# Optimization experiments

Measured on AMD Instinct MI355X. Metric: run time of the kernel, lower is better.

The kernel has to match this reference:

```python
import jax, jax.numpy as jnp
import numpy as np
from jax import lax

SIZE = 4      # pool stride / patch stride
PAD = 1       # patch halo -> window = SIZE + 2*PAD = 6
K1 = 5        # mask mixing kernel
TOPK = 240    # hard-coded number of refinement regions per batch element


def conv2d(x, w, b, pad):
    # x: [B,Cin,H,W], w: [Cout,Cin,kh,kw] (torch OIHW layout)
    y = lax.conv_general_dilated(x, w, (1, 1), [(pad, pad), (pad, pad)],
                                 dimension_numbers=("NCHW", "OIHW", "NCHW"))
    return y + b[None, :, None, None]


def setup_inputs() -> dict:
    key = jax.random.key(0)
    ks = jax.random.split(key, 7)
    B, C, H, W = 16, 50, 256, 256
    out_lr = jax.random.normal(ks[0], (B, C, H, W), dtype=jnp.float32)
    s = 0.05  # keep conv outputs / softmax numerics sane
    return {
        "out_lr": out_lr,
        "W1": jax.random.normal(ks[1], (C, C, 3, 3), jnp.float32) * s,
        "b1": jax.random.normal(ks[2], (C,), jnp.float32) * s,
        "W2": jax.random.normal(ks[3], (2, C, 3, 3), jnp.float32) * s,
        "b2": jax.random.normal(ks[4], (2,), jnp.float32) * s,
        "Wk": jax.random.normal(ks[5], (K1 * K1, 1, 1, 1), jnp.float32) * s,
        "bk": jax.random.normal(ks[6], (K1 * K1,), jnp.float32) * s,
    }


def reference(out_lr, W1, b1, W2, b2, Wk, bk):
    B, C, H, W = out_lr.shape
    Hs, Ws = H // SIZE, W // SIZE

    # spa_mask_1 Sequential: conv3x3 -> ReLU -> conv3x3 (nf -> 2 channels)
    x = jax.nn.relu(conv2d(out_lr, W1, b1, 1))
    x = conv2d(x, W2, b2, 1)                      # [B,2,H,W]

    # softmax_t over channel dim (t=1), keep channel 1
    sm = jax.nn.softmax(x, axis=1)[:, 1:2]        # [B,1,H,W]

    # adaptive_avg_pool2d to (H/4, W/4) == 4x4 avg pool (H,W divisible by SIZE)
    sm = sm.reshape(B, 1, Hs, SIZE, Ws, SIZE).mean(axis=(3, 5))  # [B,1,Hs,Ws]
    sm = jnp.where(sm >= 0, sm, 0.1 * sm)         # LeakyReLU(0.1)

    # 1x1 conv producing per-position 5x5 mixing kernel
    kern = conv2d(sm, Wk, bk, 0)[:, None]         # [B,1,25,Hs,Ws]

    # F.unfold(pad=2, kernel 5x5): 25 sliding windows in row-major (ki,kj) order
    p = (K1 - 1) // 2
    smp = jnp.pad(sm, ((0, 0), (0, 0), (p, p), (p, p)))
    windows = jnp.stack([smp[:, :, i:i + Hs, j:j + Ws]
                         for i in range(K1) for j in range(K1)], axis=2)  # [B,1,25,Hs,Ws]

    final_mask = (kern * windows).sum(axis=2)     # [B,1,Hs,Ws]

    # topk 240 per batch; scatter->nonzero in torch yields row-major sorted flat indices
    err = final_mask.reshape(B, Hs * Ws)
    _, idx = lax.top_k(err, TOPK)                 # [B,240]
    idx = jnp.sort(idx, axis=1)
    b_idx = jnp.repeat(jnp.arange(B), TOPK)       # [B*240]
    flat = idx.reshape(-1)
    h_idx = flat // Ws
    w_idx = flat % Ws

    # crop_patch: pad by 1, gather 6x6 patches at stride 4 (direct gather, no full unfold)
    padded = jnp.pad(out_lr, ((0, 0), (0, 0), (PAD, PAD), (PAD, PAD)))
    win = SIZE + 2 * PAD

    def get_patch(b, h, w):
        return lax.dynamic_slice(padded, (b, 0, h * SIZE, w * SIZE), (1, C, win, win))[0]

    patches = jax.vmap(get_patch)(b_idx, h_idx, w_idx)  # [B*240, C, 6, 6]
    return patches, b_idx, h_idx, w_idx, final_mask
```

## Files before the change

### kernel.cpp

```cpp
#include <hip/hip_runtime.h>
#include <math.h>

#define CCH   50
#define HH    256
#define WW    256
#define BATCH 16
#define HSZ   64
#define WSZ   64
#define NTOP  240
#define SPX   66
#define SROW  6

typedef __attribute__((ext_vector_type(8))) short s16x8;
typedef __attribute__((ext_vector_type(4))) float f32x4;

__device__ __forceinline__ unsigned short bf16rne(float x) {
  unsigned u = __float_as_uint(x);
  unsigned r = (u + 0x7FFFu + ((u >> 16) & 1u)) >> 16;
  return (unsigned short)r;
}
__device__ __forceinline__ float bf2f(unsigned short h) {
  return __uint_as_float(((unsigned)h) << 16);
}

__global__ __launch_bounds__(64) void prep_wfrag_k(
    const float* __restrict__ W1, unsigned short* __restrict__ wf) {
  int combo = blockIdx.x;
  int lane = threadIdx.x;
  int sp = combo & 1;
  int t2 = combo >> 1;
  int mt = t2 & 3;
  int t3 = t2 >> 2;
  int tap = t3 % 9;
  int chunk = t3 / 9;
  int co = mt * 16 + (lane & 15);
  int gbase = combo * 512 + lane * 8;
#pragma unroll
  for (int e = 0; e < 8; ++e) {
    int ci = chunk * 32 + ((lane >> 4) * 8) + e;
    float w = (co < CCH && ci < CCH) ? W1[co * (CCH * 9) + ci * 9 + tap] : 0.f;
    unsigned short h = bf16rne(w);
    unsigned short v = sp ? bf16rne(w - bf2f(h)) : h;
    wf[gbase + e] = v;
  }
}

__global__ __launch_bounds__(256, 3) void conv1_mfma_k(
    const float* __restrict__ in, const unsigned short* __restrict__ wf,
    const float* __restrict__ b1, float* __restrict__ x1p) {
  __shared__ alignas(16) short xlds[SROW * SPX * 64];

  int bx = blockIdx.x;
  int pq = bx & 3;
  int rg = (bx >> 2) & 63;
  int b  = bx >> 8;
  int row0 = rg * 4;
  int px0g = pq * 64;

  int t = threadIdx.x;
  int lane = t & 63;
  int wv = t >> 6;
  int ln15 = lane & 15;
  int lg = lane >> 4;

  f32x4 acc[4][4];
#pragma unroll
  for (int mt = 0; mt < 4; ++mt)
#pragma unroll
    for (int s = 0; s < 4; ++s) acc[mt][s] = (f32x4){0.f, 0.f, 0.f, 0.f};

  const size_t in_b = ((size_t)b * CCH) << 16;

#pragma unroll
  for (int chunk = 0; chunk < 2; ++chunk) {
    __syncthreads();
    for (int i = t; i < SROW * 4 * SPX; i += 256) {
      int ro = i / SPX;
      int px = i - ro * SPX;
      int row = ro >> 2, oct = ro & 3;
      int gr = row0 - 1 + row;
      int gx = px0g - 1 + px;
      bool okxy = (gr >= 0 && gr < HH && gx >= 0 && gx < WW);
      const float* gp = in + in_b + ((size_t)(chunk * 32 + oct * 8) << 16)
                        + (gr << 8) + gx;
      unsigned hs[8], ls[8];
#pragma unroll
      for (int e = 0; e < 8; ++e) {
        int ci = chunk * 32 + oct * 8 + e;
        float x = (okxy && ci < CCH) ? gp[(size_t)e << 16] : 0.f;
        unsigned u = __float_as_uint(x);
        unsigned hu = u & 0xFFFF0000u;
        float lo = x - __uint_as_float(hu);
        unsigned ul = __float_as_uint(lo);
        hs[e] = hu >> 16;
        ls[e] = (ul + 0x7FFFu + ((ul >> 16) & 1u)) >> 16;
      }
      s16x8 hv, lv;
#pragma unroll
      for (int e = 0; e < 8; ++e) { hv[e] = (short)hs[e]; lv[e] = (short)ls[e]; }
      int swz = (px & 7) << 3;
      int base_sh = (row * SPX + px) * 64;
      *(s16x8*)&xlds[base_sh + ((oct * 8) ^ swz)] = hv;
      *(s16x8*)&xlds[base_sh + ((32 + oct * 8) ^ swz)] = lv;
    }
    __syncthreads();

#pragma unroll
    for (int tap = 0; tap < 9; ++tap) {
      const int dh = tap / 3 - 1;
      const int dw = tap % 3 - 1;
      s16x8 ah[4], al[4];
#pragma unroll
      for (int mt = 0; mt < 4; ++mt) {
        int cb = ((chunk * 9 + tap) * 4 + mt) * 2;
        ah[mt] = *(const s16x8*)(wf + (size_t)cb * 512 + lane * 8);
        al[mt] = *(const s16x8*)(wf + (size_t)(cb + 1) * 512 + lane * 8);
      }
      int rbase = (wv + 1 + dh) * (SPX * 64);
#pragma unroll
      for (int s = 0; s < 4; ++s) {
        int pixL = 1 + s * 16 + ln15 + dw;
        int bsh = rbase + pixL * 64;
        int swz = (pixL & 7) << 3;
        s16x8 bh = *(const s16x8*)&xlds[bsh + ((lg * 8) ^ swz)];
        s16x8 bl = *(const s16x8*)&xlds[bsh + ((32 + lg * 8) ^ swz)];
        __builtin_amdgcn_s_setprio(1);
#pragma unroll
        for (int mt = 0; mt < 4; ++mt) {
          acc[mt][s] = __builtin_amdgcn_mfma_f32_16x16x32_bf16(
              ah[mt], bh, acc[mt][s], 0, 0, 0);
          acc[mt][s] = __builtin_amdgcn_mfma_f32_16x16x32_bf16(
              ah[mt], bl, acc[mt][s], 0, 0, 0);
          acc[mt][s] = __builtin_amdgcn_mfma_f32_16x16x32_bf16(
              al[mt], bh, acc[mt][s], 0, 0, 0);
        }
        __builtin_amdgcn_s_setprio(0);
      }
    }
  }

  int orow = row0 + wv;
#pragma unroll
  for (int s = 0; s < 4; ++s) {
    int px = px0g + s * 16 + ln15;
#pragma unroll
    for (int mt = 0; mt < 4; ++mt) {
#pragma unroll
      for (int reg = 0; reg < 4; ++reg) {
        int co = mt * 16 + lg * 4 + reg;
        if (co < CCH) {
          float v = fmaxf(acc[mt][s][reg] + b1[co], 0.f);
          x1p[(((size_t)b * CCH + co) << 16) + (orow << 8) + px] = v;
        }
      }
    }
  }
}

__global__ __launch_bounds__(256) void conv2_pool_k(
    const float* __restrict__ x1p, const float* __restrict__ w2,
    const float* __restrict__ b2, float* __restrict__ pool) {
  int pb = blockIdx.x;
  int l = (pb & 7) * 128 + (pb >> 3);
  int b  = l >> 6;
  int rg = l & 63;
  int row0 = rg * 4;
  int px = threadIdx.x;

  float a0, a1, a2, a3, c0, c1, c2, c3;
  a0 = a1 = a2 = a3 = b2[0];
  c0 = c1 = c2 = c3 = b2[1];
  bool wm = px > 0, wp = px < WW - 1;

  const float* xb = x1p + (((size_t)b * CCH) << 16);

#define TAP(T, A, C) { \
    A = fmaf(wc0[3 * (T)], lf, A); A = fmaf(wc0[3 * (T) + 1], m, A); \
    A = fmaf(wc0[3 * (T) + 2], rt, A); \
    C = fmaf(wc1[3 * (T)], lf, C); C = fmaf(wc1[3 * (T) + 1], m, C); \
    C = fmaf(wc1[3 * (T) + 2], rt, C); }

#define ROW(IR, BODY) { \
    int gr = row0 - 1 + (IR); \
    if (gr >= 0 && gr < HH) { \
      const float* rp = xp + (gr << 8); \
      float m  = rp[px]; \
      float lf = wm ? rp[px - 1] : 0.f; \
      float rt = wp ? rp[px + 1] : 0.f; \
      BODY \
    } }

  for (int ci = 0; ci < CCH; ++ci) {
    const float* xp = xb + ((size_t)ci << 16);
    const float* wc0 = w2 + ci * 9;
    const float* wc1 = w2 + 450 + ci * 9;
    ROW(0, TAP(0, a0, c0))
    ROW(1, TAP(0, a1, c1) TAP(1, a0, c0))
    ROW(2, TAP(0, a2, c2) TAP(1, a1, c1) TAP(2, a0, c0))
    ROW(3, TAP(0, a3, c3) TAP(1, a2, c2) TAP(2, a1, c1))
    ROW(4, TAP(1, a3, c3) TAP(2, a2, c2))
    ROW(5, TAP(2, a3, c3))
  }
#undef ROW
#undef TAP

  float s = 1.f / (1.f + expf(a0 - c0)) + 1.f / (1.f + expf(a1 - c1))
          + 1.f / (1.f + expf(a2 - c2)) + 1.f / (1.f + expf(a3 - c3));
  s += __shfl_xor(s, 1);
  s += __shfl_xor(s, 2);
  if ((px & 3) == 0) {
    float p = s * (1.f / 16.f);
    pool[(size_t)b * 4096 + rg * 64 + (px >> 2)] = (p >= 0.f) ? p : 0.1f * p;
  }
}

__global__ __launch_bounds__(1024) void mixtopk_k(
    const float* __restrict__ pool, const float* __restrict__ wk,
    const float* __restrict__ bk, float* __restrict__ mask_out,
    float* __restrict__ ob, float* __restrict__ oh, float* __restrict__ ow,
    int* __restrict__ idx_ws) {
  __shared__ unsigned long long keys[4096];
  __shared__ int sidx[256];
  int b = blockIdx.x, t = threadIdx.x;

  const float* pb = pool + (size_t)b * 4096;
  for (int i = t; i < 4096; i += 1024) {
    int hs = i >> 6, ws = i & 63;
    float c = pb[i];
    float s = 0.f;
#pragma unroll
    for (int ki = 0; ki < 5; ++ki) {
#pragma unroll
      for (int kj = 0; kj < 5; ++kj) {
        int y = hs + ki - 2, x = ws + kj - 2;
        float win = (y >= 0 && y < HSZ && x >= 0 && x < WSZ)
                        ? pb[y * WSZ + x] : 0.f;
        int k = ki * 5 + kj;
        s += (wk[k] * c + bk[k]) * win;
      }
    }
    mask_out[(size_t)b * 4096 + i] = s;
    unsigned u = __float_as_uint(s);
    u = (u & 0x80000000u) ? ~u : (u | 0x80000000u);
    u = ~u;
    keys[i] = ((unsigned long long)u << 12) | (unsigned)i;
  }
  __syncthreads();

  for (int k = 2; k <= 4096; k <<= 1) {
    for (int j = k >> 1; j > 0; j >>= 1) {
      for (int m = t; m < 2048; m += 1024) {
        int i = ((m & ~(j - 1)) << 1) | (m & (j - 1));
        int l = i | j;
        bool up = ((i & k) == 0);
        unsigned long long a = keys[i], c = keys[l];
        if ((a > c) == up) { keys[i] = c; keys[l] = a; }
      }
      __syncthreads();
    }
  }

  if (t < 256) sidx[t] = (t < NTOP) ? (int)(keys[t] & 0xFFFu) : 0x7FFFFFFF;
  __syncthreads();
  for (int k = 2; k <= 256; k <<= 1) {
    for (int j = k >> 1; j > 0; j >>= 1) {
      if (t < 128) {
        int i = ((t & ~(j - 1)) << 1) | (t & (j - 1));
        int l = i | j;
        bool up = ((i & k) == 0);
        int a = sidx[i], c = sidx[l];
        if ((a > c) == up) { sidx[i] = c; sidx[l] = a; }
      }
      __syncthreads();
    }
  }

  if (t < NTOP) {
    int id = sidx[t];
    int o = b * NTOP + t;
    ob[o] = (float)b;
    oh[o] = (float)(id >> 6);
    ow[o] = (float)(id & 63);
    idx_ws[o] = id;
  }
}

__global__ __launch_bounds__(256) void gather_patch_k(
    const float* __restrict__ in, const int* __restrict__ idx_ws,
    float* __restrict__ patches) {
  int p = blockIdx.x;
  int b = p / NTOP;
  int id = idx_ws[p];
  int h = id >> 6, w = id & 63;
  int y0 = h * 4 - 1, x0 = w * 4 - 1;
  const float* base = in + (size_t)b * CCH * 65536;
  float* op = patches + (size_t)p * (CCH * 36);
  for (int e = threadIdx.x; e < CCH * 36; e += 256) {
    int c = e / 36;
    int r = (e - c * 36) / 6;
    int col = e - c * 36 - r * 6;
    int y = y0 + r, x = x0 + col;
    float v = 0.f;
    if (y >= 0 && y < HH && x >= 0 && x < WW)
      v = base[(size_t)c * 65536 + y * WW + x];
    op[e] = v;
  }
}

extern "C" void kernel_launch(void* const* d_in, const int* in_sizes, int n_in,
                              void* d_out, int out_size, void* d_ws, size_t ws_size,
                              hipStream_t stream) {
  const float* out_lr = (const float*)d_in[0];
  const float* W1 = (const float*)d_in[1];
  const float* b1 = (const float*)d_in[2];
  const float* W2 = (const float*)d_in[3];
  const float* b2 = (const float*)d_in[4];
  const float* Wk = (const float*)d_in[5];
  const float* bk = (const float*)d_in[6];

  float* x1p  = (float*)d_ws;
  float* pool = x1p + (size_t)52428800;
  int*  idxb  = (int*)(pool + 65536);
  unsigned short* wfrag = (unsigned short*)(pool + 65536 + 3840);

  float* out    = (float*)d_out;
  float* o_patch = out;
  float* o_b    = out + (size_t)6912000;
  float* o_h    = o_b + 3840;
  float* o_w    = o_h + 3840;
  float* o_mask = o_w + 3840;

  prep_wfrag_k<<<144, 64, 0, stream>>>(W1, wfrag);
  conv1_mfma_k<<<BATCH * 64 * 4, 256, 0, stream>>>(out_lr, wfrag, b1, x1p);
  conv2_pool_k<<<BATCH * 64, 256, 0, stream>>>(x1p, W2, b2, pool);
  mixtopk_k<<<BATCH, 1024, 0, stream>>>(pool, Wk, bk, o_mask, o_b, o_h, o_w, idxb);
  gather_patch_k<<<BATCH * NTOP, 256, 0, stream>>>(out_lr, idxb, o_patch);
}
```

Before: 389.9 us.

## Switch conv1 to 32x32x16 MFMA tiles and restructure LDS layout

Conv1's implicit GEMM now uses 32x32x16 bf16 MFMA instead of 16x16x32, covering the 64 output channels with two M tiles instead of four. The weight fragment prep and the LDS activation layout (split planes per row, hi/lo and channel octet, no XOR swizzle) are changed to match. conv2_pool also moves to 512-thread blocks, each covering two 4-row groups. The aim is fewer MFMA issues and less operand traffic per FLOP. Dropping the swizzle may add LDS bank conflicts, and the larger accumulators raise register pressure.

Measured after the change: 488.1 us. 1.25x slower.

```diff
diff --git a/kernel.cpp b/kernel.cpp
--- a/kernel.cpp
+++ b/kernel.cpp
@@ -12,7 +12,7 @@
 #define SROW  6
 
 typedef __attribute__((ext_vector_type(8))) short s16x8;
-typedef __attribute__((ext_vector_type(4))) float f32x4;
+typedef __attribute__((ext_vector_type(16))) float f32x16;
 
 __device__ __forceinline__ unsigned short bf16rne(float x) {
   unsigned u = __float_as_uint(x);
@@ -28,16 +28,16 @@
   int combo = blockIdx.x;
   int lane = threadIdx.x;
   int sp = combo & 1;
-  int t2 = combo >> 1;
-  int mt = t2 & 3;
-  int t3 = t2 >> 2;
-  int tap = t3 % 9;
-  int chunk = t3 / 9;
-  int co = mt * 16 + (lane & 15);
+  int ks = (combo >> 1) & 1;
+  int mt = (combo >> 2) & 1;
+  int rest = combo >> 3;
+  int tap = rest % 9;
+  int chunk = rest / 9;
+  int co = mt * 32 + (lane & 31);
   int gbase = combo * 512 + lane * 8;
 #pragma unroll
   for (int e = 0; e < 8; ++e) {
-    int ci = chunk * 32 + ((lane >> 4) * 8) + e;
+    int ci = chunk * 32 + ks * 16 + ((lane >> 5) * 8) + e;
     float w = (co < CCH && ci < CCH) ? W1[co * (CCH * 9) + ci * 9 + tap] : 0.f;
     unsigned short h = bf16rne(w);
     unsigned short v = sp ? bf16rne(w - bf2f(h)) : h;
@@ -48,7 +48,7 @@
 __global__ __launch_bounds__(256, 3) void conv1_mfma_k(
     const float* __restrict__ in, const unsigned short* __restrict__ wf,
     const float* __restrict__ b1, float* __restrict__ x1p) {
-  __shared__ alignas(16) short xlds[SROW * SPX * 64];
+  __shared__ alignas(16) short xlds[SROW * 2 * 4 * SPX * 8];
 
   int bx = blockIdx.x;
   int pq = bx & 3;
@@ -60,14 +60,16 @@
   int t = threadIdx.x;
   int lane = t & 63;
   int wv = t >> 6;
-  int ln15 = lane & 15;
-  int lg = lane >> 4;
-
-  f32x4 acc[4][4];
-#pragma unroll
-  for (int mt = 0; mt < 4; ++mt)
-#pragma unroll
-    for (int s = 0; s < 4; ++s) acc[mt][s] = (f32x4){0.f, 0.f, 0.f, 0.f};
+  int l31 = lane & 31;
+  int lg2 = lane >> 5;
+
+  f32x16 acc[2][2];
+#pragma unroll
+  for (int mt = 0; mt < 2; ++mt)
+#pragma unroll
+    for (int pt = 0; pt < 2; ++pt)
+#pragma unroll
+      for (int r = 0; r < 16; ++r) acc[mt][pt][r] = 0.f;
 
   const size_t in_b = ((size_t)b * CCH) << 16;
 
@@ -98,10 +100,10 @@
       s16x8 hv, lv;
 #pragma unroll
       for (int e = 0; e < 8; ++e) { hv[e] = (short)hs[e]; lv[e] = (short)ls[e]; }
-      int swz = (px & 7) << 3;
-      int base_sh = (row * SPX + px) * 64;
-      *(s16x8*)&xlds[base_sh + ((oct * 8) ^ swz)] = hv;
-      *(s16x8*)&xlds[base_sh + ((32 + oct * 8) ^ swz)] = lv;
+      int bh_ = ((row * 2 + 0) * 4 + oct) * (SPX * 8) + px * 8;
+      int bl_ = ((row * 2 + 1) * 4 + oct) * (SPX * 8) + px * 8;
+      *(s16x8*)&xlds[bh_] = hv;
+      *(s16x8*)&xlds[bl_] = lv;
     }
     __syncthreads();
 
@@ -109,63 +111,70 @@
     for (int tap = 0; tap < 9; ++tap) {
       const int dh = tap / 3 - 1;
       const int dw = tap % 3 - 1;
-      s16x8 ah[4], al[4];
-#pragma unroll
-      for (int mt = 0; mt < 4; ++mt) {
-        int cb = ((chunk * 9 + tap) * 4 + mt) * 2;
-        ah[mt] = *(const s16x8*)(wf + (size_t)cb * 512 + lane * 8);
-        al[mt] = *(const s16x8*)(wf + (size_t)(cb + 1) * 512 + lane * 8);
-      }
-      int rbase = (wv + 1 + dh) * (SPX * 64);
-#pragma unroll
-      for (int s = 0; s < 4; ++s) {
-        int pixL = 1 + s * 16 + ln15 + dw;
-        int bsh = rbase + pixL * 64;
-        int swz = (pixL & 7) << 3;
-        s16x8 bh = *(const s16x8*)&xlds[bsh + ((lg * 8) ^ swz)];
-        s16x8 bl = *(const s16x8*)&xlds[bsh + ((32 + lg * 8) ^ swz)];
-        __builtin_amdgcn_s_setprio(1);
-#pragma unroll
-        for (int mt = 0; mt < 4; ++mt) {
-          acc[mt][s] = __builtin_amdgcn_mfma_f32_16x16x32_bf16(
-              ah[mt], bh, acc[mt][s], 0, 0, 0);
-          acc[mt][s] = __builtin_amdgcn_mfma_f32_16x16x32_bf16(
-              ah[mt], bl, acc[mt][s], 0, 0, 0);
-          acc[mt][s] = __builtin_amdgcn_mfma_f32_16x16x32_bf16(
-              al[mt], bh, acc[mt][s], 0, 0, 0);
+      s16x8 ah[2][2], al[2][2];
+#pragma unroll
+      for (int mt = 0; mt < 2; ++mt)
+#pragma unroll
+        for (int ks = 0; ks < 2; ++ks) {
+          int cb = (((chunk * 9 + tap) * 2 + mt) * 2 + ks) * 2;
+          ah[mt][ks] = *(const s16x8*)(wf + (size_t)cb * 512 + lane * 8);
+          al[mt][ks] = *(const s16x8*)(wf + (size_t)(cb + 1) * 512 + lane * 8);
         }
-        __builtin_amdgcn_s_setprio(0);
+      int row = wv + 1 + dh;
+#pragma unroll
+      for (int pt = 0; pt < 2; ++pt) {
+        int pixL = 1 + pt * 32 + l31 + dw;
+#pragma unroll
+        for (int ks = 0; ks < 2; ++ks) {
+          int oct = ks * 2 + lg2;
+          int hb = ((row * 2 + 0) * 4 + oct) * (SPX * 8) + pixL * 8;
+          int lb = ((row * 2 + 1) * 4 + oct) * (SPX * 8) + pixL * 8;
+          s16x8 bh = *(const s16x8*)&xlds[hb];
+          s16x8 bl = *(const s16x8*)&xlds[lb];
+          __builtin_amdgcn_s_setprio(1);
+#pragma unroll
+          for (int mt = 0; mt < 2; ++mt) {
+            acc[mt][pt] = __builtin_amdgcn_mfma_f32_32x32x16_bf16(
+                ah[mt][ks], bh, acc[mt][pt], 0, 0, 0);
+            acc[mt][pt] = __builtin_amdgcn_mfma_f32_32x32x16_bf16(
+                ah[mt][ks], bl, acc[mt][pt], 0, 0, 0);
+            acc[mt][pt] = __builtin_amdgcn_mfma_f32_32x32x16_bf16(
+                al[mt][ks], bh, acc[mt][pt], 0, 0, 0);
+          }
+          __builtin_amdgcn_s_setprio(0);
+        }
       }
     }
   }
 
   int orow = row0 + wv;
 #pragma unroll
-  for (int s = 0; s < 4; ++s) {
-    int px = px0g + s * 16 + ln15;
-#pragma unroll
-    for (int mt = 0; mt < 4; ++mt) {
-#pragma unroll
-      for (int reg = 0; reg < 4; ++reg) {
-        int co = mt * 16 + lg * 4 + reg;
+  for (int mt = 0; mt < 2; ++mt)
+#pragma unroll
+    for (int pt = 0; pt < 2; ++pt) {
+      int px = px0g + pt * 32 + l31;
+#pragma unroll
+      for (int reg = 0; reg < 16; ++reg) {
+        int co = mt * 32 + (reg & 3) + 8 * (reg >> 2) + 4 * lg2;
         if (co < CCH) {
-          float v = fmaxf(acc[mt][s][reg] + b1[co], 0.f);
+          float v = fmaxf(acc[mt][pt][reg] + b1[co], 0.f);
           x1p[(((size_t)b * CCH + co) << 16) + (orow << 8) + px] = v;
         }
       }
     }
-  }
-}
-
-__global__ __launch_bounds__(256) void conv2_pool_k(
+}
+
+__global__ __launch_bounds__(512) void conv2_pool_k(
     const float* __restrict__ x1p, const float* __restrict__ w2,
     const float* __restrict__ b2, float* __restrict__ pool) {
   int pb = blockIdx.x;
-  int l = (pb & 7) * 128 + (pb >> 3);
-  int b  = l >> 6;
-  int rg = l & 63;
-  int row0 = rg * 4;
-  int px = threadIdx.x;
+  int l = (pb & 7) * 64 + (pb >> 3);
+  int b  = l >> 5;
+  int rg = l & 31;
+  int t = threadIdx.x;
+  int px = t & 255;
+  int half = t >> 8;
+  int row0 = rg * 8 + half * 4;
 
   float a0, a1, a2, a3, c0, c1, c2, c3;
   a0 = a1 = a2 = a3 = b2[0];
@@ -210,7 +219,8 @@
   s += __shfl_xor(s, 2);
   if ((px & 3) == 0) {
     float p = s * (1.f / 16.f);
-    pool[(size_t)b * 4096 + rg * 64 + (px >> 2)] = (p >= 0.f) ? p : 0.1f * p;
+    pool[(size_t)b * 4096 + (rg * 2 + half) * 64 + (px >> 2)] =
+        (p >= 0.f) ? p : 0.1f * p;
   }
 }
 
@@ -332,7 +342,7 @@
 
   prep_wfrag_k<<<144, 64, 0, stream>>>(W1, wfrag);
   conv1_mfma_k<<<BATCH * 64 * 4, 256, 0, stream>>>(out_lr, wfrag, b1, x1p);
-  conv2_pool_k<<<BATCH * 64, 256, 0, stream>>>(x1p, W2, b2, pool);
+  conv2_pool_k<<<BATCH * 32, 512, 0, stream>>>(x1p, W2, b2, pool);
   mixtopk_k<<<BATCH, 1024, 0, stream>>>(pool, Wk, bk, o_mask, o_b, o_h, o_w, idxb);
   gather_patch_k<<<BATCH * NTOP, 256, 0, stream>>>(out_lr, idxb, o_patch);
 }
```

## Prefetch second channel chunk into registers while computing first chunk MFMAs

Applied to the files above, without the earlier changes.

The conv1 kernel now issues the global loads for the second 32-channel chunk into a 56-float register array before running the first chunk's tap MFMAs. It converts and writes that data to LDS afterwards. The aim is to hide global load latency behind tensor-core work instead of stalling at a barrier between chunks. In exchange, register pressure rises considerably, which may lower occupancy or cause spills.

Result: slower. 425.7 us (+9.2%).

```diff
diff --git a/kernel.cpp b/kernel.cpp
--- a/kernel.cpp
+++ b/kernel.cpp
@@ -10,6 +10,7 @@
 #define NTOP  240
 #define SPX   66
 #define SROW  6
+#define NITEM (SROW * 4 * SPX)
 
 typedef __attribute__((ext_vector_type(8))) short s16x8;
 typedef __attribute__((ext_vector_type(4))) float f32x4;
@@ -71,73 +72,118 @@
 
   const size_t in_b = ((size_t)b * CCH) << 16;
 
-#pragma unroll
-  for (int chunk = 0; chunk < 2; ++chunk) {
-    __syncthreads();
-    for (int i = t; i < SROW * 4 * SPX; i += 256) {
+#define CONVERT_WRITE(i, xv)                                            \
+  {                                                                     \
+    int ro = (i) / SPX;                                                 \
+    int px = (i) - ro * SPX;                                            \
+    int row = ro >> 2, oct = ro & 3;                                    \
+    unsigned hs[8], ls[8];                                              \
+    _Pragma("unroll")                                                   \
+    for (int e = 0; e < 8; ++e) {                                       \
+      float x = xv[e];                                                  \
+      unsigned u = __float_as_uint(x);                                  \
+      unsigned hu = u & 0xFFFF0000u;                                    \
+      float lo = x - __uint_as_float(hu);                               \
+      unsigned ul = __float_as_uint(lo);                                \
+      hs[e] = hu >> 16;                                                 \
+      ls[e] = (ul + 0x7FFFu + ((ul >> 16) & 1u)) >> 16;                 \
+    }                                                                   \
+    s16x8 hv, lv;                                                       \
+    _Pragma("unroll")                                                   \
+    for (int e = 0; e < 8; ++e) {                                       \
+      hv[e] = (short)hs[e]; lv[e] = (short)ls[e];                       \
+    }                                                                   \
+    int swz = (px & 7) << 3;                                            \
+    int base_sh = (row * SPX + px) * 64;                                \
+    *(s16x8*)&xlds[base_sh + ((oct * 8) ^ swz)] = hv;                   \
+    *(s16x8*)&xlds[base_sh + ((32 + oct * 8) ^ swz)] = lv;              \
+  }
+
+#define TAPS(chunk)                                                     \
+  _Pragma("unroll")                                                     \
+  for (int tap = 0; tap < 9; ++tap) {                                   \
+    const int dh = tap / 3 - 1;                                         \
+    const int dw = tap % 3 - 1;                                         \
+    s16x8 ah[4], al[4];                                                 \
+    _Pragma("unroll")                                                   \
+    for (int mt = 0; mt < 4; ++mt) {                                    \
+      int cb = (((chunk) * 9 + tap) * 4 + mt) * 2;                      \
+      ah[mt] = *(const s16x8*)(wf + (size_t)cb * 512 + lane * 8);       \
+      al[mt] = *(const s16x8*)(wf + (size_t)(cb + 1) * 512 + lane * 8); \
+    }                                                                   \
+    int rbase = (wv + 1 + dh) * (SPX * 64);                             \
+    _Pragma("unroll")                                                   \
+    for (int s = 0; s < 4; ++s) {                                       \
+      int pixL = 1 + s * 16 + ln15 + dw;                                \
+      int bsh = rbase + pixL * 64;                                      \
+      int swz = (pixL & 7) << 3;                                        \
+      s16x8 bh = *(const s16x8*)&xlds[bsh + ((lg * 8) ^ swz)];          \
+      s16x8 bl = *(const s16x8*)&xlds[bsh + ((32 + lg * 8) ^ swz)];     \
+      __builtin_amdgcn_s_setprio(1);                                    \
+      _Pragma("unroll")                                                 \
+      for (int mt = 0; mt < 4; ++mt) {                                  \
+        acc[mt][s] = __builtin_amdgcn_mfma_f32_16x16x32_bf16(           \
+            ah[mt], bh, acc[mt][s], 0, 0, 0);                           \
+        acc[mt][s] = __builtin_amdgcn_mfma_f32_16x16x32_bf16(           \
+            ah[mt], bl, acc[mt][s], 0, 0, 0);                           \
+        acc[mt][s] = __builtin_amdgcn_mfma_f32_16x16x32_bf16(           \
+            al[mt], bh, acc[mt][s], 0, 0, 0);                           \
+      }                                                                 \
+      __builtin_amdgcn_s_setprio(0);                                    \
+    }                                                                   \
+  }
+
+  for (int i = t; i < NITEM; i += 256) {
+    int ro = i / SPX;
+    int px = i - ro * SPX;
+    int row = ro >> 2, oct = ro & 3;
+    int gr = row0 - 1 + row;
+    int gx = px0g - 1 + px;
+    bool okxy = (gr >= 0 && gr < HH && gx >= 0 && gx < WW);
+    const float* gp = in + in_b + ((size_t)(oct * 8) << 16) + (gr << 8) + gx;
+    float xv[8];
+#pragma unroll
+    for (int e = 0; e < 8; ++e)
+      xv[e] = okxy ? gp[(size_t)e << 16] : 0.f;
+    CONVERT_WRITE(i, xv)
+  }
+  __syncthreads();
+
+  float pre[7][8];
+#pragma unroll
+  for (int it = 0; it < 7; ++it) {
+    int i = t + it * 256;
+    if (i < NITEM) {
       int ro = i / SPX;
       int px = i - ro * SPX;
       int row = ro >> 2, oct = ro & 3;
       int gr = row0 - 1 + row;
       int gx = px0g - 1 + px;
       bool okxy = (gr >= 0 && gr < HH && gx >= 0 && gx < WW);
-      const float* gp = in + in_b + ((size_t)(chunk * 32 + oct * 8) << 16)
+      const float* gp = in + in_b + ((size_t)(32 + oct * 8) << 16)
                         + (gr << 8) + gx;
-      unsigned hs[8], ls[8];
 #pragma unroll
       for (int e = 0; e < 8; ++e) {
-        int ci = chunk * 32 + oct * 8 + e;
-        float x = (okxy && ci < CCH) ? gp[(size_t)e << 16] : 0.f;
-        unsigned u = __float_as_uint(x);
-        unsigned hu = u & 0xFFFF0000u;
-        float lo = x - __uint_as_float(hu);
-        unsigned ul = __float_as_uint(lo);
-        hs[e] = hu >> 16;
-        ls[e] = (ul + 0x7FFFu + ((ul >> 16) & 1u)) >> 16;
-      }
-      s16x8 hv, lv;
-#pragma unroll
-      for (int e = 0; e < 8; ++e) { hv[e] = (short)hs[e]; lv[e] = (short)ls[e]; }
-      int swz = (px & 7) << 3;
-      int base_sh = (row * SPX + px) * 64;
-      *(s16x8*)&xlds[base_sh + ((oct * 8) ^ swz)] = hv;
-      *(s16x8*)&xlds[base_sh + ((32 + oct * 8) ^ swz)] = lv;
-    }
-    __syncthreads();
-
-#pragma unroll
-    for (int tap = 0; tap < 9; ++tap) {
-      const int dh = tap / 3 - 1;
-      const int dw = tap % 3 - 1;
-      s16x8 ah[4], al[4];
-#pragma unroll
-      for (int mt = 0; mt < 4; ++mt) {
-        int cb = ((chunk * 9 + tap) * 4 + mt) * 2;
-        ah[mt] = *(const s16x8*)(wf + (size_t)cb * 512 + lane * 8);
-        al[mt] = *(const s16x8*)(wf + (size_t)(cb + 1) * 512 + lane * 8);
-      }
-      int rbase = (wv + 1 + dh) * (SPX * 64);
-#pragma unroll
-      for (int s = 0; s < 4; ++s) {
-        int pixL = 1 + s * 16 + ln15 + dw;
-        int bsh = rbase + pixL * 64;
-        int swz = (pixL & 7) << 3;
-        s16x8 bh = *(const s16x8*)&xlds[bsh + ((lg * 8) ^ swz)];
-        s16x8 bl = *(const s16x8*)&xlds[bsh + ((32 + lg * 8) ^ swz)];
-        __builtin_amdgcn_s_setprio(1);
-#pragma unroll
-        for (int mt = 0; mt < 4; ++mt) {
-          acc[mt][s] = __builtin_amdgcn_mfma_f32_16x16x32_bf16(
-              ah[mt], bh, acc[mt][s], 0, 0, 0);
-          acc[mt][s] = __builtin_amdgcn_mfma_f32_16x16x32_bf16(
-              ah[mt], bl, acc[mt][s], 0, 0, 0);
-          acc[mt][s] = __builtin_amdgcn_mfma_f32_16x16x32_bf16(
-              al[mt], bh, acc[mt][s], 0, 0, 0);
-        }
-        __builtin_amdgcn_s_setprio(0);
-      }
-    }
-  }
+        int ci = 32 + oct * 8 + e;
+        pre[it][e] = (okxy && ci < CCH) ? gp[(size_t)e << 16] : 0.f;
+      }
+    }
+  }
+
+  TAPS(0)
+  __syncthreads();
+
+#pragma unroll
+  for (int it = 0; it < 7; ++it) {
+    int i = t + it * 256;
+    if (i < NITEM) CONVERT_WRITE(i, pre[it])
+  }
+  __syncthreads();
+
+  TAPS(1)
+
+#undef TAPS
+#undef CONVERT_WRITE
 
   int orow = row0 + wv;
 #pragma unroll
```
